# Optimization experiments

Hardware: AMD Instinct MI355X
Metric: run time of the kernel (lower is better)

Reference implementation:

```python
import jax, jax.numpy as jnp
import numpy as np

N_NODES = 100000
D_IN = 64
D_OUT = 64
N_EDGES = 1250000


def setup_inputs() -> dict:
    key = jax.random.key(0)
    k_x, k_e, k_wl, k_bl, k_wr = jax.random.split(key, 5)
    x = jax.random.normal(k_x, (N_NODES, D_IN), dtype=jnp.float32)
    edge_index = jax.random.randint(k_e, (2, N_EDGES), 0, N_NODES, dtype=jnp.int64)
    # SAGEConv params: lin_l (neighbor transform, with bias), lin_r (root transform, no bias)
    s_in = 1.0 / np.sqrt(D_IN)
    W_l = jax.random.uniform(k_wl, (D_IN, D_OUT), dtype=jnp.float32, minval=-s_in, maxval=s_in)
    b_l = jax.random.uniform(k_bl, (D_OUT,), dtype=jnp.float32, minval=-s_in, maxval=s_in)
    W_r = jax.random.uniform(k_wr, (D_IN, D_OUT), dtype=jnp.float32, minval=-s_in, maxval=s_in)
    return {"x": x, "edge_index": edge_index, "W_l": W_l, "b_l": b_l, "W_r": W_r}


def reference(x, edge_index, W_l, b_l, W_r):
    # PyG SAGEConv with aggr='add':
    #   out = lin_l(sum_{j in N(i)} x_j) + lin_r(x_i), then tanh
    src = edge_index[0]  # message sources (x_j)
    dst = edge_index[1]  # message targets (i)
    msg = x[src]                                             # [E, D_IN] gather
    aggr = jax.ops.segment_sum(msg, dst, num_segments=x.shape[0])  # [N, D_IN] scatter-add
    out = aggr @ W_l + b_l + x @ W_r                         # [N, D_OUT]
    return jnp.tanh(out)
```

## Files before the change

### kernel.cpp

```cpp
#include <hip/hip_runtime.h>
#include <hip/hip_bf16.h>
#include <hip/hip_fp16.h>

#define N_NODES 100000
#define D 64
#define N_EDGES 1250000

#define RB 64
#define NB 1563
#define FCAP 1536
#define SORT_CAP 1536

#define CB_SHIFT 11
#define NCB 49
#define CCAP 28672
#define FINE_PER_COARSE 32

#define EPB 8192
#define PARTA_BLOCKS ((N_EDGES + EPB - 1) / EPB)
#define SEGS 8

#define TN 64
#define PRE_BLOCKS 1563
#define FUSED_BLOCKS (PARTA_BLOCKS + PRE_BLOCKS)

#define XP 72

typedef unsigned short ushort_t;
typedef _Float16 half_t;
typedef __attribute__((ext_vector_type(8))) _Float16 half8;
typedef __attribute__((ext_vector_type(4))) float floatx4;

__global__ __launch_bounds__(256) void pre_part_kernel(
    const float* __restrict__ x, const float* __restrict__ W_l,
    const float* __restrict__ b_l, const float* __restrict__ W_r,
    ushort_t* __restrict__ y, ushort_t* __restrict__ z,
    const int* __restrict__ src, const int* __restrict__ dst,
    int* __restrict__ ccursor, unsigned* __restrict__ coarse,
    int N, int E)
{
    int t = threadIdx.x;

    if (blockIdx.x < PARTA_BLOCKS) {
        __shared__ int hist[NCB];
        __shared__ int bbase[NCB];
        if (t < NCB) hist[t] = 0;
        __syncthreads();

        int base = blockIdx.x * EPB;
        int lim = E - base; if (lim > EPB) lim = EPB;

        for (int i = t; i < lim; i += 256) {
            int d = dst[base + i];
            atomicAdd(&hist[d >> CB_SHIFT], 1);
        }
        __syncthreads();

        if (t < NCB) {
            int c = hist[t];
            bbase[t] = c ? atomicAdd(&ccursor[t], c) : 0;
        }
        __syncthreads();

        for (int i = t; i < lim; i += 256) {
            int d = dst[base + i];
            int s = src[base + i];
            int b = d >> CB_SHIFT;
            int pos = atomicSub(&hist[b], 1) - 1;
            coarse[(size_t)b * CCAP + bbase[b] + pos] =
                (unsigned)s | ((unsigned)(d & ((1 << CB_SHIFT) - 1)) << 17);
        }
        return;
    }

    __shared__ half_t sWt[128 * XP];
    __shared__ half_t sXh[TN * XP];

    for (int i = t; i < 64 * 64; i += 256) {
        int k = i >> 6, c = i & 63;
        sWt[c * XP + k]        = (half_t)W_l[i];
        sWt[(64 + c) * XP + k] = (half_t)W_r[i];
    }

    long base = (long)(blockIdx.x - PARTA_BLOCKS) * TN;
    for (int i = t; i < TN * 16; i += 256) {
        int n = i >> 4, q = i & 15;
        long node = base + n;
        float4 v = make_float4(0.f, 0.f, 0.f, 0.f);
        if (node < N) v = ((const float4*)(x + node * D))[q];
        half_t* p = &sXh[n * XP + q * 4];
        p[0] = (half_t)v.x; p[1] = (half_t)v.y;
        p[2] = (half_t)v.z; p[3] = (half_t)v.w;
    }
    __syncthreads();

    const int lane  = t & 63;
    const int w     = t >> 6;
    const int col16 = lane & 15;
    const int quad  = lane >> 4;

    const int nrow = w * 16 + col16;
    half8 a0 = *(half8*)&sXh[nrow * XP + quad * 8];
    half8 a1 = *(half8*)&sXh[nrow * XP + 32 + quad * 8];

    float bias[4];
#pragma unroll
    for (int j = 0; j < 4; j++) bias[j] = b_l[j * 16 + col16];

    long nodeBase = base + w * 16;

#pragma unroll 2
    for (int ct = 0; ct < 8; ct++) {
        int c = ct * 16 + col16;
        half8 b0 = *(half8*)&sWt[c * XP + quad * 8];
        half8 b1 = *(half8*)&sWt[c * XP + 32 + quad * 8];
        floatx4 acc = {0.f, 0.f, 0.f, 0.f};
        acc = __builtin_amdgcn_mfma_f32_16x16x32_f16(a0, b0, acc, 0, 0, 0);
        acc = __builtin_amdgcn_mfma_f32_16x16x32_f16(a1, b1, acc, 0, 0, 0);

        ushort_t* obuf = (ct < 4) ? y : z;
        int cc    = (ct < 4) ? c : (c - 64);
        float badd = (ct < 4) ? 0.f : bias[ct - 4];
#pragma unroll
        for (int r = 0; r < 4; r++) {
            long node = nodeBase + quad * 4 + r;
            if (node < N) {
                half_t hv = (half_t)(acc[r] + badd);
                obuf[node * D + cc] = *(ushort_t*)&hv;
            }
        }
    }
}

__global__ __launch_bounds__(256) void partB_kernel(
    const unsigned* __restrict__ coarse, const int* __restrict__ ccursor,
    int* __restrict__ fcursor, unsigned* __restrict__ fine)
{
    __shared__ int hist[FINE_PER_COARSE];
    __shared__ int bbase[FINE_PER_COARSE];
    int cb = blockIdx.x >> 3;
    int seg = blockIdx.x & 7;
    int t = threadIdx.x;

    int cnt = ccursor[cb];
    int segLen = (cnt + SEGS - 1) / SEGS;
    int beg = seg * segLen;
    int end = beg + segLen; if (end > cnt) end = cnt;

    if (t < FINE_PER_COARSE) hist[t] = 0;
    __syncthreads();

    const unsigned* __restrict__ slab = coarse + (size_t)cb * CCAP;

    for (int i = beg + t; i < end; i += 256) {
        unsigned e = slab[i];
        atomicAdd(&hist[(e >> 17) >> 6], 1);
    }
    __syncthreads();

    if (t < FINE_PER_COARSE) {
        int c = hist[t];
        int fb = cb * FINE_PER_COARSE + t;
        bbase[t] = c ? atomicAdd(&fcursor[fb], c) : 0;
    }
    __syncthreads();

    for (int i = beg + t; i < end; i += 256) {
        unsigned e = slab[i];
        unsigned cl = e >> 17;
        int fb_loc = cl >> 6;
        int pos = atomicSub(&hist[fb_loc], 1) - 1;
        size_t fb = (size_t)cb * FINE_PER_COARSE + fb_loc;
        fine[fb * FCAP + bbase[fb_loc] + pos] =
            (e & 0x1FFFFu) | ((cl & 63u) << 17);
    }
}

__global__ __launch_bounds__(512) void sortgather_kernel(
    const ushort_t* __restrict__ y, const ushort_t* __restrict__ z,
    const unsigned* __restrict__ part, const int* __restrict__ cursor,
    float* __restrict__ out, int N)
{
    __shared__ int sorted[SORT_CAP];
    __shared__ int hist[RB];
    __shared__ int scanv[RB];
    __shared__ int cur[RB];
    __shared__ int begL[RB];

    int b = blockIdx.x;
    int t = threadIdx.x;
    int cnt = cursor[b];
    if (cnt > SORT_CAP) cnt = SORT_CAP;
    const unsigned* __restrict__ slab = part + (size_t)b * FCAP;

    unsigned e0 = 0, e1 = 0, e2 = 0;
    int i0 = t, i1 = t + 512, i2 = t + 1024;
    if (i0 < cnt) e0 = slab[i0];
    if (i1 < cnt) e1 = slab[i1];
    if (i2 < cnt) e2 = slab[i2];

    if (t < RB) hist[t] = 0;
    __syncthreads();

    if (i0 < cnt) atomicAdd(&hist[e0 >> 17], 1);
    if (i1 < cnt) atomicAdd(&hist[e1 >> 17], 1);
    if (i2 < cnt) atomicAdd(&hist[e2 >> 17], 1);
    __syncthreads();

    if (t < RB) scanv[t] = hist[t];
    __syncthreads();
#pragma unroll
    for (int off = 1; off < RB; off <<= 1) {
        int v = 0;
        if (t < RB && t >= off) v = scanv[t - off];
        __syncthreads();
        if (t < RB) scanv[t] += v;
        __syncthreads();
    }
    if (t < RB) {
        int ex = scanv[t] - hist[t];
        cur[t] = ex;
        begL[t] = ex;
    }
    __syncthreads();

    if (i0 < cnt) { int p = atomicAdd(&cur[e0 >> 17], 1); sorted[p] = (int)(e0 & 0x1FFFF); }
    if (i1 < cnt) { int p = atomicAdd(&cur[e1 >> 17], 1); sorted[p] = (int)(e1 & 0x1FFFF); }
    if (i2 < cnt) { int p = atomicAdd(&cur[e2 >> 17], 1); sorted[p] = (int)(e2 & 0x1FFFF); }
    __syncthreads();

    const int g = t >> 3;
    const int f = t & 7;
    int myBeg = begL[g];
    int myDeg = hist[g];

    float2 acc0 = make_float2(0.f, 0.f), acc1 = acc0, acc2 = acc0, acc3 = acc0;

    int i = 0;
    for (; i + 4 <= myDeg; i += 4) {
        int s0 = sorted[myBeg + i];
        int s1 = sorted[myBeg + i + 1];
        int s2 = sorted[myBeg + i + 2];
        int s3 = sorted[myBeg + i + 3];
        uint4 r0 = ((const uint4*)(y + (size_t)s0 * D))[f];
        uint4 r1 = ((const uint4*)(y + (size_t)s1 * D))[f];
        uint4 r2 = ((const uint4*)(y + (size_t)s2 * D))[f];
        uint4 r3 = ((const uint4*)(y + (size_t)s3 * D))[f];
#define ACC(r) { \
        float2 c0 = __half22float2(*(const __half2*)&(r).x); \
        float2 c1 = __half22float2(*(const __half2*)&(r).y); \
        float2 c2 = __half22float2(*(const __half2*)&(r).z); \
        float2 c3 = __half22float2(*(const __half2*)&(r).w); \
        acc0.x += c0.x; acc0.y += c0.y; acc1.x += c1.x; acc1.y += c1.y; \
        acc2.x += c2.x; acc2.y += c2.y; acc3.x += c3.x; acc3.y += c3.y; }
        ACC(r0) ACC(r1) ACC(r2) ACC(r3)
    }
    for (; i < myDeg; i++) {
        int s = sorted[myBeg + i];
        uint4 r = ((const uint4*)(y + (size_t)s * D))[f];
        ACC(r)
    }
#undef ACC

    long gn = (long)b * RB + g;
    if (gn < N) {
        uint4 zr = ((const uint4*)(z + (size_t)gn * D))[f];
        float2 z0 = __half22float2(*(const __half2*)&zr.x);
        float2 z1 = __half22float2(*(const __half2*)&zr.y);
        float2 z2 = __half22float2(*(const __half2*)&zr.z);
        float2 z3 = __half22float2(*(const __half2*)&zr.w);
        float4 o0, o1;
        o0.x = tanhf(acc0.x + z0.x); o0.y = tanhf(acc0.y + z0.y);
        o0.z = tanhf(acc1.x + z1.x); o0.w = tanhf(acc1.y + z1.y);
        o1.x = tanhf(acc2.x + z2.x); o1.y = tanhf(acc2.y + z2.y);
        o1.z = tanhf(acc3.x + z3.x); o1.w = tanhf(acc3.y + z3.y);
        float4* op = (float4*)(out + gn * D);
        op[2 * f] = o0;
        op[2 * f + 1] = o1;
    }
}

extern "C" void kernel_launch(void* const* d_in, const int* in_sizes, int n_in,
                              void* d_out, int out_size, void* d_ws, size_t ws_size,
                              hipStream_t stream) {
    const float* x   = (const float*)d_in[0];
    const int* ei    = (const int*)d_in[1];
    const float* W_l = (const float*)d_in[2];
    const float* b_l = (const float*)d_in[3];
    const float* W_r = (const float*)d_in[4];
    float* out = (float*)d_out;

    const int N = N_NODES;
    const int E = N_EDGES;
    const int* src = ei;
    const int* dst = ei + E;

    char* ws = (char*)d_ws;
    ushort_t* y      = (ushort_t*)(ws);
    ushort_t* z      = (ushort_t*)(ws + 12800000);
    unsigned* coarse = (unsigned*)(ws + 25600000);
    unsigned* fine   = (unsigned*)(ws + 31219712);
    int* ccursor     = (int*)(ws + 40822784);
    int* fcursor     = (int*)(ws + 40823040);

    hipMemsetAsync(ccursor, 0, 6508, stream);

    pre_part_kernel<<<FUSED_BLOCKS, 256, 0, stream>>>(
        x, W_l, b_l, W_r, y, z, src, dst, ccursor, coarse, N, E);
    partB_kernel<<<NCB * SEGS, 256, 0, stream>>>(coarse, ccursor, fcursor, fine);
    sortgather_kernel<<<NB, 512, 0, stream>>>(y, z, fine, fcursor, out, N);
}
```

Baseline: 149.9 us.

## Privatize per-wave histograms, shrink partition chunks, use wave-shuffle scan

```diff
diff --git a/kernel.cpp b/kernel.cpp
--- a/kernel.cpp
+++ b/kernel.cpp
@@ -16,9 +16,9 @@
 #define CCAP 28672
 #define FINE_PER_COARSE 32
 
-#define EPB 8192
+#define EPB 2048
 #define PARTA_BLOCKS ((N_EDGES + EPB - 1) / EPB)
-#define SEGS 8
+#define SEGS 16
 
 #define TN 64
 #define PRE_BLOCKS 1563
@@ -42,9 +42,11 @@
     int t = threadIdx.x;
 
     if (blockIdx.x < PARTA_BLOCKS) {
-        __shared__ int hist[NCB];
-        __shared__ int bbase[NCB];
-        if (t < NCB) hist[t] = 0;
+        __shared__ int hist[4][NCB];
+        __shared__ int wbase[4][NCB];
+        const int w = t >> 6;
+
+        if (t < 4 * NCB) ((int*)hist)[t] = 0;
         __syncthreads();
 
         int base = blockIdx.x * EPB;
@@ -52,13 +54,19 @@
 
         for (int i = t; i < lim; i += 256) {
             int d = dst[base + i];
-            atomicAdd(&hist[d >> CB_SHIFT], 1);
+            atomicAdd(&hist[w][d >> CB_SHIFT], 1);
         }
         __syncthreads();
 
         if (t < NCB) {
-            int c = hist[t];
-            bbase[t] = c ? atomicAdd(&ccursor[t], c) : 0;
+            int c0 = hist[0][t], c1 = hist[1][t];
+            int c2 = hist[2][t], c3 = hist[3][t];
+            int tot = c0 + c1 + c2 + c3;
+            int b0 = tot ? atomicAdd(&ccursor[t], tot) : 0;
+            wbase[0][t] = b0;
+            wbase[1][t] = b0 + c0;
+            wbase[2][t] = b0 + c0 + c1;
+            wbase[3][t] = b0 + c0 + c1 + c2;
         }
         __syncthreads();
 
@@ -66,8 +74,8 @@
             int d = dst[base + i];
             int s = src[base + i];
             int b = d >> CB_SHIFT;
-            int pos = atomicSub(&hist[b], 1) - 1;
-            coarse[(size_t)b * CCAP + bbase[b] + pos] =
+            int pos = atomicSub(&hist[w][b], 1) - 1;
+            coarse[(size_t)b * CCAP + wbase[w][b] + pos] =
                 (unsigned)s | ((unsigned)(d & ((1 << CB_SHIFT) - 1)) << 17);
         }
         return;
@@ -136,32 +144,39 @@
     const unsigned* __restrict__ coarse, const int* __restrict__ ccursor,
     int* __restrict__ fcursor, unsigned* __restrict__ fine)
 {
-    __shared__ int hist[FINE_PER_COARSE];
-    __shared__ int bbase[FINE_PER_COARSE];
-    int cb = blockIdx.x >> 3;
-    int seg = blockIdx.x & 7;
+    __shared__ int hist[4][FINE_PER_COARSE];
+    __shared__ int wbase[4][FINE_PER_COARSE];
+    int cb = blockIdx.x >> 4;
+    int seg = blockIdx.x & 15;
     int t = threadIdx.x;
+    const int w = t >> 6;
 
     int cnt = ccursor[cb];
     int segLen = (cnt + SEGS - 1) / SEGS;
     int beg = seg * segLen;
     int end = beg + segLen; if (end > cnt) end = cnt;
 
-    if (t < FINE_PER_COARSE) hist[t] = 0;
+    if (t < 4 * FINE_PER_COARSE) ((int*)hist)[t] = 0;
     __syncthreads();
 
     const unsigned* __restrict__ slab = coarse + (size_t)cb * CCAP;
 
     for (int i = beg + t; i < end; i += 256) {
         unsigned e = slab[i];
-        atomicAdd(&hist[(e >> 17) >> 6], 1);
+        atomicAdd(&hist[w][(e >> 17) >> 6], 1);
     }
     __syncthreads();
 
     if (t < FINE_PER_COARSE) {
-        int c = hist[t];
+        int c0 = hist[0][t], c1 = hist[1][t];
+        int c2 = hist[2][t], c3 = hist[3][t];
+        int tot = c0 + c1 + c2 + c3;
         int fb = cb * FINE_PER_COARSE + t;
-        bbase[t] = c ? atomicAdd(&fcursor[fb], c) : 0;
+        int b0 = tot ? atomicAdd(&fcursor[fb], tot) : 0;
+        wbase[0][t] = b0;
+        wbase[1][t] = b0 + c0;
+        wbase[2][t] = b0 + c0 + c1;
+        wbase[3][t] = b0 + c0 + c1 + c2;
     }
     __syncthreads();
 
@@ -169,9 +184,9 @@
         unsigned e = slab[i];
         unsigned cl = e >> 17;
         int fb_loc = cl >> 6;
-        int pos = atomicSub(&hist[fb_loc], 1) - 1;
+        int pos = atomicSub(&hist[w][fb_loc], 1) - 1;
         size_t fb = (size_t)cb * FINE_PER_COARSE + fb_loc;
-        fine[fb * FCAP + bbase[fb_loc] + pos] =
+        fine[fb * FCAP + wbase[w][fb_loc] + pos] =
             (e & 0x1FFFFu) | ((cl & 63u) << 17);
     }
 }
@@ -183,7 +198,6 @@
 {
     __shared__ int sorted[SORT_CAP];
     __shared__ int hist[RB];
-    __shared__ int scanv[RB];
     __shared__ int cur[RB];
     __shared__ int begL[RB];
 
@@ -207,18 +221,15 @@
     if (i2 < cnt) atomicAdd(&hist[e2 >> 17], 1);
     __syncthreads();
 
-    if (t < RB) scanv[t] = hist[t];
-    __syncthreads();
+    if (t < RB) {
+        int v = hist[t];
+        int inc = v;
 #pragma unroll
-    for (int off = 1; off < RB; off <<= 1) {
-        int v = 0;
-        if (t < RB && t >= off) v = scanv[t - off];
-        __syncthreads();
-        if (t < RB) scanv[t] += v;
-        __syncthreads();
-    }
-    if (t < RB) {
-        int ex = scanv[t] - hist[t];
+        for (int off = 1; off < RB; off <<= 1) {
+            int n = __shfl_up(inc, off, RB);
+            if (t >= off) inc += n;
+        }
+        int ex = inc - v;
         cur[t] = ex;
         begL[t] = ex;
     }
```

After: 149.7 us. No clear change (-0.2%).
